# Performance work log

Measured on AMD Instinct MI355X. Metric: run time of the kernel, lower is better.

The kernel has to match this reference:

```python
import jax, jax.numpy as jnp
import numpy as np

# Module hyperparameters (from init_kwargs)
KH = KW = 3
STRIDE = 2
PAD = 1
OUT_PAD = 1
DIL = 1
IN_LEN = 8   # length of each input capsule
OUT_LEN = 8  # length of each output capsule
N_IN_CAPS = 64 // IN_LEN    # 8
N_OUT_CAPS = 64 // OUT_LEN  # 8
NUM_ITERATIONS = 3


def _squash(x):
    # v * |v|^2 / ((1 + |v|^2) * |v|), along last (capsule-length) dim
    sn = jnp.sum(x * x, axis=-1, keepdims=True)
    return x * (sn / ((1.0 + sn) * jnp.sqrt(sn + 1e-12)))


def _k_means_routing(priors, num_iterations):
    # priors: [..., K, M] ; soft k-means routing with 'dot' similarity,
    # softmax over the votes dim K (softmax_dim=-2), squash at the end.
    out = jnp.mean(priors, axis=-2, keepdims=True)          # [..., 1, M]
    for _ in range(num_iterations):
        nrm = jnp.linalg.norm(out, axis=-1, keepdims=True)
        out_n = out / jnp.maximum(nrm, 1e-12)               # F.normalize(p=2)
        logits = jnp.sum(priors * out_n, axis=-1, keepdims=True)  # [..., K, 1]
        probs = jax.nn.softmax(logits, axis=-2)
        out = jnp.sum(probs * priors, axis=-2, keepdims=True)
    return _squash(out)[..., 0, :]                          # [..., M]


def setup_inputs() -> dict:
    key = jax.random.key(0)
    k1, k2, k3 = jax.random.split(key, 3)
    input = jax.random.normal(k1, (2, 64, 32, 32), dtype=jnp.float32)
    # weight: (in_length, out_channels//out_length, out_length, kh, kw)
    weight = jax.random.normal(k2, (IN_LEN, N_OUT_CAPS, OUT_LEN, KH, KW), dtype=jnp.float32) * 0.1
    # bias: (out_channels//out_length, out_length)
    bias = jax.random.normal(k3, (N_OUT_CAPS, OUT_LEN), dtype=jnp.float32) * 0.1
    return {"input": input, "weight": weight, "bias": bias}


def reference(input, weight, bias):
    n, c_in, h_in, w_in = input.shape
    fi = c_in // IN_LEN
    fo = weight.shape[1]
    # conv_transpose == conv(lhs-dilated input, spatially flipped kernel)
    pad_lo = DIL * (KH - 1) - PAD
    patches = jax.lax.conv_general_dilated_patches(
        input, (KH, KW), (1, 1),
        padding=((pad_lo, pad_lo + OUT_PAD), (pad_lo, pad_lo + OUT_PAD)),
        lhs_dilation=(STRIDE, STRIDE), rhs_dilation=(DIL, DIL))
    ho, wo = patches.shape[-2], patches.shape[-1]
    # feature dim of patches is ordered (c, kh, kw), channel-major
    patches = patches.reshape(n, fi, IN_LEN, KH, KW, ho, wo)
    w_flip = weight[..., ::-1, ::-1]  # [IN_LEN, fo, OUT_LEN, KH, KW]
    # votes: each (input capsule, kernel tap) casts a vote per output capsule
    priors = jnp.einsum('nflhwpq,lgmhw->npqgfhwm', patches, w_flip)
    priors = priors.reshape(n, ho, wo, fo, fi * KH * KW, OUT_LEN)
    out = _k_means_routing(priors, NUM_ITERATIONS)  # [n, ho, wo, fo, OUT_LEN]
    out = out + bias                                # bias: [fo, OUT_LEN]
    out = out.reshape(n, ho, wo, fo * OUT_LEN).transpose(0, 3, 1, 2)
    return out  # [n, out_channels, ho, wo] = [2, 64, 64, 64]
```

## Files before the change

kernel.cpp:

```cpp
#include <hip/hip_runtime.h>
#include <math.h>

#define HIN 32
#define WIN 32
#define NITER 3

typedef float f2 __attribute__((ext_vector_type(2)));
__device__ __forceinline__ f2 mk2(float a, float b) { f2 r; r.x = a; r.y = b; return r; }
__device__ __forceinline__ f2 fma2(f2 a, f2 b, f2 c) { return __builtin_elementwise_fma(a, b, c); }

template <int CTRL>
__device__ __forceinline__ float dpp_add(float v) {
    int p = __builtin_amdgcn_update_dpp(0, __float_as_int(v), CTRL, 0xF, 0xF, true);
    return v + __int_as_float(p);
}
__device__ __forceinline__ float sum8(float v) {
    v = dpp_add<0xB1>(v);
    v = dpp_add<0x4E>(v);
    v = dpp_add<0x141>(v);
    return v;
}

template <int TH, int TW>
__device__ __forceinline__ void run_path(
    const float* __restrict__ weight, const float* __restrict__ bias,
    float* __restrict__ out, const float* __restrict__ ilds,
    float* __restrict__ wlds, float* __restrict__ olds,
    int t, int n, int p, int qb, int x0) {
    constexpr int T = TH * TW;
    constexpr float Z = (float)(72 - 8 * T);

    {
        const int sg = (t >> 3) & 7;
        const int sm = t & 7;
        const int l0 = t >> 6;
        const int dbase = sg * 80 + (((sm >> 1) + sg) & 3) * 20 + (sm & 1);
#pragma unroll
        for (int k = 0; k < 2 * T; ++k) {
            const int vtap = k >> 1;
            const int chunk = k & 1;
            const int hh = (TH == 1) ? 1 : ((vtap / TW) * 2);
            const int ww = (TW == 1) ? 1 : ((vtap % TW) * 2);
            const int jflip = (2 - hh) * 3 + (2 - ww);
            const int l = chunk * 4 + l0;
            wlds[vtap * 640 + dbase + l * 2] =
                weight[(chunk * 256 + t) * 9 + jflip];
        }
    }
    __syncthreads();

    const int wave = t >> 6;
    const int lane = t & 63;
    const int g = lane >> 3;
    const int s = lane & 7;
    const int q = qb + 2 * wave;

    f2 pri2[T][4];
#pragma unroll
    for (int i = 0; i < TH; ++i) {
        const int h = (TH == 1) ? 1 : i * 2;
        const int y = (p + h - 1) >> 1;
#pragma unroll
        for (int j = 0; j < TW; ++j) {
            const int v = i * TW + j;
            const int w = (TW == 1) ? 1 : j * 2;
            const int x = (q + w - 1) >> 1;
            const bool valid = (y < HIN) && (x < WIN);
            if (valid) {
                const float4* xp =
                    (const float4*)(ilds + ((i * 8) + (x - x0)) * 64 + s * 8);
                float4 x0v = xp[0], x1v = xp[1];
                float xv[8] = {x0v.x, x0v.y, x0v.z, x0v.w, x1v.x, x1v.y, x1v.z, x1v.w};
                const float* wb = wlds + v * 640 + g * 80;
#pragma unroll
                for (int m2 = 0; m2 < 4; ++m2) {
                    const float4* row = (const float4*)(wb + ((m2 + g) & 3) * 20);
                    f2 acc = mk2(0.f, 0.f);
#pragma unroll
                    for (int k = 0; k < 4; ++k) {
                        float4 w4 = row[k];
                        acc = fma2(mk2(xv[2 * k], xv[2 * k]), mk2(w4.x, w4.y), acc);
                        acc = fma2(mk2(xv[2 * k + 1], xv[2 * k + 1]), mk2(w4.z, w4.w), acc);
                    }
                    pri2[v][m2] = acc;
                }
            } else {
#pragma unroll
                for (int m2 = 0; m2 < 4; ++m2) pri2[v][m2] = mk2(0.f, 0.f);
            }
        }
    }

    f2 rr[4];
#pragma unroll
    for (int m2 = 0; m2 < 4; ++m2) {
        f2 a = mk2(0.f, 0.f);
#pragma unroll
        for (int v = 0; v < T; ++v) a += pri2[v][m2];
        rr[m2].x = sum8(a.x);
        rr[m2].y = sum8(a.y);
    }

    float r8v = 0.f;
#pragma unroll
    for (int it = 0; it < NITER; ++it) {
        f2 t2 = mk2(0.f, 0.f);
#pragma unroll
        for (int m2 = 0; m2 < 4; ++m2) t2 = fma2(rr[m2], rr[m2], t2);
        const float sn = t2.x + t2.y;
        const float inv = __builtin_amdgcn_rsqf(fmaxf(sn, 1e-24f));
        const f2 inv2 = mk2(inv, inv);
        f2 on2[4];
#pragma unroll
        for (int m2 = 0; m2 < 4; ++m2) on2[m2] = rr[m2] * inv2;

        float a8 = 0.f;
        f2 acc2[4];
#pragma unroll
        for (int m2 = 0; m2 < 4; ++m2) acc2[m2] = mk2(0.f, 0.f);
#pragma unroll
        for (int v = 0; v < T; ++v) {
            f2 d2 = mk2(0.f, 0.f);
#pragma unroll
            for (int m2 = 0; m2 < 4; ++m2) d2 = fma2(pri2[v][m2], on2[m2], d2);
            const float e = __expf(d2.x + d2.y);
            a8 += e;
            const f2 e2 = mk2(e, e);
#pragma unroll
            for (int m2 = 0; m2 < 4; ++m2) acc2[m2] = fma2(e2, pri2[v][m2], acc2[m2]);
        }
#pragma unroll
        for (int m2 = 0; m2 < 4; ++m2) {
            rr[m2].x = sum8(acc2[m2].x);
            rr[m2].y = sum8(acc2[m2].y);
        }
        if (it == NITER - 1) r8v = sum8(a8);
    }

    const float invs = __builtin_amdgcn_rcpf(r8v + Z);
    const f2 invs2 = mk2(invs, invs);
    f2 o2[4];
#pragma unroll
    for (int m2 = 0; m2 < 4; ++m2) o2[m2] = rr[m2] * invs2;

    f2 s2 = mk2(0.f, 0.f);
#pragma unroll
    for (int m2 = 0; m2 < 4; ++m2) s2 = fma2(o2[m2], o2[m2], s2);
    const float sn = s2.x + s2.y;
    const float factor =
        sn * __builtin_amdgcn_rcpf(1.f + sn) * __builtin_amdgcn_rsqf(sn + 1e-12f);

    f2 osel = o2[0];
#pragma unroll
    for (int m2 = 1; m2 < 4; ++m2)
        if ((s >> 1) == m2) osel = o2[m2];
    float val = (s & 1) ? osel.y : osel.x;
    val = val * factor + bias[g * 8 + s];

    olds[lane * 5 + wave] = val;

    __syncthreads();
    const int c2 = t >> 2, w = t & 3;
    out[(((size_t)n * 64 + c2) * 64 + p) * 64 + qb + 2 * w] = olds[c2 * 5 + w];
}

__global__ __launch_bounds__(256) void caps_routing(
    const float* __restrict__ in, const float* __restrict__ weight,
    const float* __restrict__ bias, float* __restrict__ out) {
    __shared__ float ilds[2 * 8 * 64];
    __shared__ float wlds[4 * 640];
    __shared__ float olds[64 * 5];
    const int t = threadIdx.x;

    const int b = blockIdx.x;
    const int n = b >> 10;
    const int p = (b >> 4) & 63;
    const int j = b & 15;
    const int qpar = j >> 3;
    const int qb = (j & 7) * 8 + qpar;
    const int x0 = (j & 7) * 4;
    const int y0 = p >> 1;
    const int nrows = (p & 1) ? 2 : 1;

    {
        const int c = t >> 2, r = t & 3;
        const int yi = r >> 1, f4 = r & 1;
        const int chunk = x0 + f4 * 4;
        const int y = y0 + yi;
        float4 vv = {0.f, 0.f, 0.f, 0.f};
        if (yi < nrows && y < HIN && chunk < WIN)
            vv = *(const float4*)(in + (((size_t)(n * 64 + c) * HIN + y) * WIN + chunk));
        ilds[(yi * 8 + f4 * 4 + 0) * 64 + c] = vv.x;
        ilds[(yi * 8 + f4 * 4 + 1) * 64 + c] = vv.y;
        ilds[(yi * 8 + f4 * 4 + 2) * 64 + c] = vv.z;
        ilds[(yi * 8 + f4 * 4 + 3) * 64 + c] = vv.w;
    }

    if (p & 1) {
        if (qpar)
            run_path<2, 2>(weight, bias, out, ilds, wlds, olds, t, n, p, qb, x0);
        else
            run_path<2, 1>(weight, bias, out, ilds, wlds, olds, t, n, p, qb, x0);
    } else {
        if (qpar)
            run_path<1, 2>(weight, bias, out, ilds, wlds, olds, t, n, p, qb, x0);
        else
            run_path<1, 1>(weight, bias, out, ilds, wlds, olds, t, n, p, qb, x0);
    }
}

extern "C" void kernel_launch(void* const* d_in, const int* in_sizes, int n_in,
                              void* d_out, int out_size, void* d_ws, size_t ws_size,
                              hipStream_t stream) {
    const float* in = (const float*)d_in[0];
    const float* weight = (const float*)d_in[1];
    const float* bias = (const float*)d_in[2];
    float* out = (float*)d_out;
    (void)d_ws; (void)ws_size;

    caps_routing<<<2048, 256, 0, stream>>>(in, weight, bias, out);
}
```

Baseline: 68.37 us.

## Rebalance work: lighter tap-count blocks process two output columns per thread

Blocks are reassigned so that parity classes with fewer kernel taps (1 or 2 taps) handle two output pixels per thread, while the 4-tap class keeps one. The grid shrinks from 2048 to 1280 blocks with roughly uniform work per block. This also amortizes weight and input staging across more outputs. The dual paths double register use for priors, which may hurt occupancy.

```diff
diff --git a/kernel.cpp b/kernel.cpp
--- a/kernel.cpp
+++ b/kernel.cpp
@@ -6,8 +6,8 @@
 #define NITER 3
 
 typedef float f2 __attribute__((ext_vector_type(2)));
-__device__ __forceinline__ f2 mk2(float a, float b) { f2 r; r.x = a; r.y = b; return r; }
-__device__ __forceinline__ f2 fma2(f2 a, f2 b, f2 c) { return __builtin_elementwise_fma(a, b, c); }
+static __device__ __forceinline__ f2 mk2(float a, float b) { f2 r; r.x = a; r.y = b; return r; }
+static __device__ __forceinline__ f2 fma2(f2 a, f2 b, f2 c) { return __builtin_elementwise_fma(a, b, c); }
 
 template <int CTRL>
 __device__ __forceinline__ float dpp_add(float v) {
@@ -22,53 +22,62 @@
 }
 
 template <int TH, int TW>
-__device__ __forceinline__ void run_path(
-    const float* __restrict__ weight, const float* __restrict__ bias,
-    float* __restrict__ out, const float* __restrict__ ilds,
-    float* __restrict__ wlds, float* __restrict__ olds,
-    int t, int n, int p, int qb, int x0) {
+__device__ __forceinline__ void stage_weights(const float* __restrict__ weight,
+                                              float* __restrict__ wlds, int t) {
     constexpr int T = TH * TW;
-    constexpr float Z = (float)(72 - 8 * T);
-
-    {
-        const int sg = (t >> 3) & 7;
-        const int sm = t & 7;
-        const int l0 = t >> 6;
-        const int dbase = sg * 80 + (((sm >> 1) + sg) & 3) * 20 + (sm & 1);
-#pragma unroll
-        for (int k = 0; k < 2 * T; ++k) {
-            const int vtap = k >> 1;
-            const int chunk = k & 1;
-            const int hh = (TH == 1) ? 1 : ((vtap / TW) * 2);
-            const int ww = (TW == 1) ? 1 : ((vtap % TW) * 2);
-            const int jflip = (2 - hh) * 3 + (2 - ww);
-            const int l = chunk * 4 + l0;
-            wlds[vtap * 640 + dbase + l * 2] =
-                weight[(chunk * 256 + t) * 9 + jflip];
-        }
-    }
-    __syncthreads();
-
-    const int wave = t >> 6;
-    const int lane = t & 63;
-    const int g = lane >> 3;
-    const int s = lane & 7;
-    const int q = qb + 2 * wave;
-
-    f2 pri2[T][4];
+    const int sg = (t >> 3) & 7;
+    const int sm = t & 7;
+    const int l0 = t >> 6;
+    const int dbase = sg * 80 + (((sm >> 1) + sg) & 3) * 20 + (sm & 1);
+#pragma unroll
+    for (int k = 0; k < 2 * T; ++k) {
+        const int vtap = k >> 1;
+        const int chunk = k & 1;
+        const int hh = (TH == 1) ? 1 : ((vtap / TW) * 2);
+        const int ww = (TW == 1) ? 1 : ((vtap % TW) * 2);
+        const int jflip = (2 - hh) * 3 + (2 - ww);
+        const int l = chunk * 4 + l0;
+        wlds[vtap * 640 + dbase + l * 2] = weight[(chunk * 256 + t) * 9 + jflip];
+    }
+}
+
+template <int NROWS, int NCHUNK>
+__device__ __forceinline__ void stage_input(const float* __restrict__ in,
+                                            float* __restrict__ ilds,
+                                            int t, int n, int y0, int x0) {
+    const int c = t >> 2, r = t & 3;
+#pragma unroll
+    for (int pp = r; pp < NROWS * NCHUNK; pp += 4) {
+        const int yi = pp / NCHUNK, ch = pp % NCHUNK;
+        const int y = y0 + yi;
+        const int xc = x0 + ch * 4;
+        float4 vv = {0.f, 0.f, 0.f, 0.f};
+        if (y < HIN && xc < WIN)
+            vv = *(const float4*)(in + (((size_t)(n * 64 + c) * HIN + y) * WIN + xc));
+        ilds[(yi * 12 + ch * 4 + 0) * 64 + c] = vv.x;
+        ilds[(yi * 12 + ch * 4 + 1) * 64 + c] = vv.y;
+        ilds[(yi * 12 + ch * 4 + 2) * 64 + c] = vv.z;
+        ilds[(yi * 12 + ch * 4 + 3) * 64 + c] = vv.w;
+    }
+}
+
+template <int TH, int TW>
+__device__ __forceinline__ void compute_pri(const float* __restrict__ ilds,
+                                            const float* __restrict__ wlds,
+                                            int q, int x0, int pi, int g, int s,
+                                            f2 (&pri2)[TH * TW][4]) {
 #pragma unroll
     for (int i = 0; i < TH; ++i) {
-        const int h = (TH == 1) ? 1 : i * 2;
-        const int y = (p + h - 1) >> 1;
+        const int y = (TH == 1) ? pi : (pi + i);
+        const bool vy = (y < HIN);
 #pragma unroll
         for (int j = 0; j < TW; ++j) {
             const int v = i * TW + j;
             const int w = (TW == 1) ? 1 : j * 2;
             const int x = (q + w - 1) >> 1;
-            const bool valid = (y < HIN) && (x < WIN);
-            if (valid) {
+            if (vy && x < WIN) {
                 const float4* xp =
-                    (const float4*)(ilds + ((i * 8) + (x - x0)) * 64 + s * 8);
+                    (const float4*)(ilds + (i * 12 + (x - x0)) * 64 + s * 8);
                 float4 x0v = xp[0], x1v = xp[1];
                 float xv[8] = {x0v.x, x0v.y, x0v.z, x0v.w, x1v.x, x1v.y, x1v.z, x1v.w};
                 const float* wb = wlds + v * 640 + g * 80;
@@ -90,7 +99,13 @@
             }
         }
     }
-
+}
+
+template <int T>
+__device__ __forceinline__ float route_core(const f2 (&pri2)[T][4],
+                                            const float* __restrict__ bias,
+                                            int g, int s) {
+    constexpr float Z = (float)(72 - 8 * T);
     f2 rr[4];
 #pragma unroll
     for (int m2 = 0; m2 < 4; ++m2) {
@@ -100,7 +115,6 @@
         rr[m2].x = sum8(a.x);
         rr[m2].y = sum8(a.y);
     }
-
     float r8v = 0.f;
 #pragma unroll
     for (int it = 0; it < NITER; ++it) {
@@ -136,29 +150,77 @@
         }
         if (it == NITER - 1) r8v = sum8(a8);
     }
-
     const float invs = __builtin_amdgcn_rcpf(r8v + Z);
     const f2 invs2 = mk2(invs, invs);
     f2 o2[4];
 #pragma unroll
     for (int m2 = 0; m2 < 4; ++m2) o2[m2] = rr[m2] * invs2;
-
     f2 s2 = mk2(0.f, 0.f);
 #pragma unroll
     for (int m2 = 0; m2 < 4; ++m2) s2 = fma2(o2[m2], o2[m2], s2);
     const float sn = s2.x + s2.y;
     const float factor =
         sn * __builtin_amdgcn_rcpf(1.f + sn) * __builtin_amdgcn_rsqf(sn + 1e-12f);
-
     f2 osel = o2[0];
 #pragma unroll
     for (int m2 = 1; m2 < 4; ++m2)
         if ((s >> 1) == m2) osel = o2[m2];
     float val = (s & 1) ? osel.y : osel.x;
-    val = val * factor + bias[g * 8 + s];
-
-    olds[lane * 5 + wave] = val;
-
+    return val * factor + bias[g * 8 + s];
+}
+
+template <int TH, int TW>
+__device__ __forceinline__ void run_dual(
+    const float* __restrict__ in, const float* __restrict__ weight,
+    const float* __restrict__ bias, float* __restrict__ out,
+    float* __restrict__ ilds, float* __restrict__ wlds, float* __restrict__ olds,
+    int t, int n, int p, int pi, int qb, int x0) {
+    constexpr int T = TH * TW;
+    stage_input<TH, (TW == 2 ? 3 : 2)>(in, ilds, t, n, pi, x0);
+    stage_weights<TH, TW>(weight, wlds, t);
+    __syncthreads();
+
+    const int wave = t >> 6;
+    const int lane = t & 63;
+    const int g = lane >> 3;
+    const int s = lane & 7;
+    const int qa = qb + 2 * wave;
+
+    f2 pa[T][4], pb[T][4];
+    compute_pri<TH, TW>(ilds, wlds, qa, x0, pi, g, s, pa);
+    compute_pri<TH, TW>(ilds, wlds, qa + 8, x0, pi, g, s, pb);
+
+    const float va = route_core<T>(pa, bias, g, s);
+    const float vb = route_core<T>(pb, bias, g, s);
+
+    olds[lane * 9 + wave] = va;
+    olds[lane * 9 + wave + 4] = vb;
+    __syncthreads();
+    const int c2 = t >> 2, w = t & 3;
+    float* ob = out + (((size_t)n * 64 + c2) * 64 + p) * 64 + qb;
+    ob[2 * w] = olds[c2 * 9 + w];
+    ob[2 * w + 8] = olds[c2 * 9 + w + 4];
+}
+
+__device__ __forceinline__ void run_t4(
+    const float* __restrict__ in, const float* __restrict__ weight,
+    const float* __restrict__ bias, float* __restrict__ out,
+    float* __restrict__ ilds, float* __restrict__ wlds, float* __restrict__ olds,
+    int t, int n, int p, int pi, int qb, int x0) {
+    stage_input<2, 2>(in, ilds, t, n, pi, x0);
+    stage_weights<2, 2>(weight, wlds, t);
+    __syncthreads();
+
+    const int wave = t >> 6;
+    const int lane = t & 63;
+    const int g = lane >> 3;
+    const int s = lane & 7;
+
+    f2 pa[4][4];
+    compute_pri<2, 2>(ilds, wlds, qb + 2 * wave, x0, pi, g, s, pa);
+    const float va = route_core<4>(pa, bias, g, s);
+
+    olds[lane * 5 + wave] = va;
     __syncthreads();
     const int c2 = t >> 2, w = t & 3;
     out[(((size_t)n * 64 + c2) * 64 + p) * 64 + qb + 2 * w] = olds[c2 * 5 + w];
@@ -167,45 +229,33 @@
 __global__ __launch_bounds__(256) void caps_routing(
     const float* __restrict__ in, const float* __restrict__ weight,
     const float* __restrict__ bias, float* __restrict__ out) {
-    __shared__ float ilds[2 * 8 * 64];
+    __shared__ float ilds[2 * 12 * 64];
     __shared__ float wlds[4 * 640];
-    __shared__ float olds[64 * 5];
+    __shared__ float olds[576];
     const int t = threadIdx.x;
 
     const int b = blockIdx.x;
-    const int n = b >> 10;
-    const int p = (b >> 4) & 63;
-    const int j = b & 15;
-    const int qpar = j >> 3;
-    const int qb = (j & 7) * 8 + qpar;
-    const int x0 = (j & 7) * 4;
-    const int y0 = p >> 1;
-    const int nrows = (p & 1) ? 2 : 1;
-
-    {
-        const int c = t >> 2, r = t & 3;
-        const int yi = r >> 1, f4 = r & 1;
-        const int chunk = x0 + f4 * 4;
-        const int y = y0 + yi;
-        float4 vv = {0.f, 0.f, 0.f, 0.f};
-        if (yi < nrows && y < HIN && chunk < WIN)
-            vv = *(const float4*)(in + (((size_t)(n * 64 + c) * HIN + y) * WIN + chunk));
-        ilds[(yi * 8 + f4 * 4 + 0) * 64 + c] = vv.x;
-        ilds[(yi * 8 + f4 * 4 + 1) * 64 + c] = vv.y;
-        ilds[(yi * 8 + f4 * 4 + 2) * 64 + c] = vv.z;
-        ilds[(yi * 8 + f4 * 4 + 3) * 64 + c] = vv.w;
-    }
-
-    if (p & 1) {
-        if (qpar)
-            run_path<2, 2>(weight, bias, out, ilds, wlds, olds, t, n, p, qb, x0);
+    const int grp = b / 5;
+    const int sel = b - grp * 5;
+
+    if (sel < 2) {
+        const int idx = grp * 2 + sel;
+        const int n = idx >> 8, r = idx & 255;
+        const int pi = r >> 3, jq = r & 7;
+        run_t4(in, weight, bias, out, ilds, wlds, olds,
+               t, n, 2 * pi + 1, pi, 8 * jq + 1, 4 * jq);
+    } else {
+        const int n = grp >> 7, r = grp & 127;
+        const int pi = r >> 2, jq = r & 3;
+        if (sel == 2)
+            run_dual<2, 1>(in, weight, bias, out, ilds, wlds, olds,
+                           t, n, 2 * pi + 1, pi, 16 * jq, 8 * jq);
+        else if (sel == 3)
+            run_dual<1, 2>(in, weight, bias, out, ilds, wlds, olds,
+                           t, n, 2 * pi, pi, 16 * jq + 1, 8 * jq);
         else
-            run_path<2, 1>(weight, bias, out, ilds, wlds, olds, t, n, p, qb, x0);
-    } else {
-        if (qpar)
-            run_path<1, 2>(weight, bias, out, ilds, wlds, olds, t, n, p, qb, x0);
-        else
-            run_path<1, 1>(weight, bias, out, ilds, wlds, olds, t, n, p, qb, x0);
+            run_dual<1, 1>(in, weight, bias, out, ilds, wlds, olds,
+                           t, n, 2 * pi, pi, 16 * jq, 8 * jq);
     }
 }
 
@@ -218,5 +268,5 @@
     float* out = (float*)d_out;
     (void)d_ws; (void)ws_size;
 
-    caps_routing<<<2048, 256, 0, stream>>>(in, weight, bias, out);
-}
+    caps_routing<<<1280, 256, 0, stream>>>(in, weight, bias, out);
+}
```

After: 66.76 us (median of 2 runs). 2.4% less time.
